# Kernel tuning notes

Hardware: AMD Instinct MI355X
Metric: run time of the kernel (lower is better)

## Reference

```python
import jax, jax.numpy as jnp
import numpy as np

DIM = 128
HID = 128
EPS = 1e-5

def setup_inputs() -> dict:
    key = jax.random.key(0)
    ks = jax.random.split(key, 9)
    s = 1.0 / np.sqrt(DIM)
    sh = 1.0 / np.sqrt(HID)
    return {
        "pair_repr": jax.random.normal(ks[0], (1, 512, 512, DIM), dtype=jnp.float32),
        "Wl": jax.random.uniform(ks[1], (DIM, HID), jnp.float32, -s, s),
        "bl": jax.random.uniform(ks[2], (HID,), jnp.float32, -s, s),
        "Wr": jax.random.uniform(ks[3], (DIM, HID), jnp.float32, -s, s),
        "br": jax.random.uniform(ks[4], (HID,), jnp.float32, -s, s),
        "Wo": jax.random.uniform(ks[5], (HID, DIM), jnp.float32, -sh, sh),
        "bo": jax.random.uniform(ks[6], (DIM,), jnp.float32, -sh, sh),
        "Wg": jax.random.uniform(ks[7], (DIM, DIM), jnp.float32, -s, s),
        "bg": jax.random.uniform(ks[8], (DIM,), jnp.float32, -s, s),
        "gamma": jnp.ones((DIM,), jnp.float32),
        "beta": jnp.zeros((DIM,), jnp.float32),
    }

def reference(pair_repr, Wl, bl, Wr, br, Wo, bo, Wg, bg, gamma, beta):
    # left/right projections: (B, L, L, H)
    left = pair_repr @ Wl + bl
    right = pair_repr @ Wr + br
    # triangle multiplication: out[b,i,j,h] = sum_k left[b,i,k,h] * right[b,k,j,h]
    out = jnp.einsum('bikh,bkjh->bijh', left, right)
    out = out @ Wo + bo
    gate = jax.nn.sigmoid(pair_repr @ Wg + bg)
    out = pair_repr + gate * out
    # LayerNorm over last dim
    mu = jnp.mean(out, axis=-1, keepdims=True)
    var = jnp.mean((out - mu) ** 2, axis=-1, keepdims=True)
    return (out - mu) * jax.lax.rsqrt(var + EPS) * gamma + beta
```

## Files before the change

kernel.cpp:

```cpp
#include <hip/hip_runtime.h>
#include <hip/hip_bf16.h>


#define LSZ 512
#define NPOS (LSZ * LSZ)

typedef short s16;
typedef __attribute__((ext_vector_type(4))) short s16x4;
typedef __attribute__((ext_vector_type(8))) short s16x8;
typedef __attribute__((ext_vector_type(4))) float f32x4;

typedef const __attribute__((address_space(1))) unsigned int* gas1;
typedef __attribute__((address_space(3))) unsigned int* las3;

static __device__ __forceinline__ s16 f2bf(float f) {
    unsigned int u = __builtin_bit_cast(unsigned int, f);
    u += 0x7FFFu + ((u >> 16) & 1u);
    return (s16)(u >> 16);
}

static __device__ __forceinline__ unsigned pkbf(float x, float y) {
    __hip_bfloat162 h = __float22bfloat162_rn(make_float2(x, y));
    unsigned u;
    __builtin_memcpy(&u, &h, 4);
    return u;
}
static __device__ __forceinline__ s16x8 cvt8(f32x4 a, f32x4 b) {
    union { s16x8 v; unsigned u[4]; } r;
    r.u[0] = pkbf(a[0], a[1]);
    r.u[1] = pkbf(a[2], a[3]);
    r.u[2] = pkbf(b[0], b[1]);
    r.u[3] = pkbf(b[2], b[3]);
    return r.v;
}
static __device__ __forceinline__ s16x4 cvt4(float x0, float x1, float x2, float x3) {
    union { s16x4 v; unsigned u[2]; } r;
    r.u[0] = pkbf(x0, x1);
    r.u[1] = pkbf(x2, x3);
    return r.v;
}

static __device__ __forceinline__ void gload_lds16(const void* g, void* l) {
    __builtin_amdgcn_global_load_lds((gas1)g, (las3)l, 16, 0, 0);
}

__global__ void k_prep(const float* __restrict__ Wl, const float* __restrict__ Wr,
                       const float* __restrict__ Wg, const float* __restrict__ Wo,
                       s16* __restrict__ WlT, s16* __restrict__ WrT,
                       s16* __restrict__ WgT, s16* __restrict__ WoT) {
    const float* src;
    s16* dst;
    switch (blockIdx.x) {
        case 0: src = Wl; dst = WlT; break;
        case 1: src = Wr; dst = WrT; break;
        case 2: src = Wg; dst = WgT; break;
        default: src = Wo; dst = WoT; break;
    }
    for (int e = threadIdx.x; e < 128 * 128; e += blockDim.x) {
        int o = e >> 7, i = e & 127;
        dst[e] = f2bf(src[i * 128 + o]);
    }
}

template <int COLMODE>
__global__ __launch_bounds__(256) void k_proj(const float* __restrict__ pair,
                                              const s16* __restrict__ WT,
                                              const float* __restrict__ bias,
                                              s16* __restrict__ outT) {
    __shared__ __align__(16) s16 As[128 * 128];
    const int t = threadIdx.x;
    const int b = blockIdx.x;
    const int c0 = b & 511, rb = b >> 9;
    {
        const int p = t >> 1;
        const int dh = (t & 1) << 6;
        long gpos = COLMODE ? ((long)(rb * 128 + p) * 512 + c0) : ((long)b * 128 + p);
        const float* src = pair + gpos * 128 + dh;
        const int swz = (p & 7) << 4;
        char* lrow = (char*)As + p * 256;
#pragma unroll
        for (int g = 0; g < 8; ++g) {
            f32x4 v0 = *(const f32x4*)(src + g * 8);
            f32x4 v1 = *(const f32x4*)(src + g * 8 + 4);
            s16x8 pk = cvt8(v0, v1);
            *(s16x8*)(lrow + ((dh * 2 + g * 16) ^ swz)) = pk;
        }
    }
    __syncthreads();
    const int w = t >> 6, l = t & 63;
    const int wr = (w >> 1) * 64, wc = (w & 1) * 64;
    const int lr = l & 15, lg = l >> 4;
    f32x4 acc[4][4];
#pragma unroll
    for (int mi = 0; mi < 4; ++mi)
#pragma unroll
        for (int ni = 0; ni < 4; ++ni) acc[mi][ni] = (f32x4){0.f, 0.f, 0.f, 0.f};
#pragma unroll
    for (int ks = 0; ks < 4; ++ks) {
        const int kk = ks * 32 + lg * 8;
        s16x8 af[4], bfv[4];
#pragma unroll
        for (int mi = 0; mi < 4; ++mi) {
            int row = wr + mi * 16 + lr;
            af[mi] = *(const s16x8*)((const char*)As + ((row * 256 + kk * 2) ^ ((row & 7) << 4)));
        }
#pragma unroll
        for (int ni = 0; ni < 4; ++ni) {
            int h = wc + ni * 16 + lr;
            bfv[ni] = *(const s16x8*)(WT + h * 128 + kk);
        }
#pragma unroll
        for (int mi = 0; mi < 4; ++mi)
#pragma unroll
            for (int ni = 0; ni < 4; ++ni)
                acc[mi][ni] = __builtin_amdgcn_mfma_f32_16x16x32_bf16(af[mi], bfv[ni], acc[mi][ni], 0, 0, 0);
    }
#pragma unroll
    for (int ni = 0; ni < 4; ++ni) {
        const int h = wc + ni * 16 + lr;
        const float bv = bias[h];
        long base = (long)h * NPOS + (COLMODE ? ((long)c0 * 512 + rb * 128) : ((long)b * 128));
#pragma unroll
        for (int mi = 0; mi < 4; ++mi) {
            const int prow = wr + mi * 16 + lg * 4;
            s16x4 pk = cvt4(acc[mi][ni][0] + bv, acc[mi][ni][1] + bv,
                            acc[mi][ni][2] + bv, acc[mi][ni][3] + bv);
            *(s16x4*)(outT + base + prow) = pk;
        }
    }
}

__global__ __launch_bounds__(512, 2) void k_tri(const s16* __restrict__ leftT,
                                                const s16* __restrict__ rightTT,
                                                s16* __restrict__ tri) {
    __shared__ __align__(16) s16 As[256 * 64];
    __shared__ __align__(16) s16 Bs[256 * 64];
    const int t = threadIdx.x;
    const int logical = ((blockIdx.x & 7) << 6) | (blockIdx.x >> 3);
    const int h = logical >> 2;
    const int ti = (logical >> 1) & 1, tj = logical & 1;
    const s16* Ap = leftT + (long)h * NPOS + (long)ti * 256 * 512;
    const s16* Bp = rightTT + (long)h * NPOS + (long)tj * 256 * 512;
    const int w = t >> 6, l = t & 63;
    const int wr = (w >> 2) * 128, wc = (w & 3) * 64;
    const int lr = l & 15, lg = l >> 4;
    f32x4 acc[8][4];
#pragma unroll
    for (int mi = 0; mi < 8; ++mi)
#pragma unroll
        for (int ni = 0; ni < 4; ++ni) acc[mi][ni] = (f32x4){0.f, 0.f, 0.f, 0.f};
    for (int kb = 0; kb < 512; kb += 64) {
        __syncthreads();
#pragma unroll
        for (int P = 0; P < 4; ++P) {
            const int unit = P * 512 + t;
            const int row = unit >> 3, u = unit & 7;
            const int kks = (u ^ (row & 7)) << 3;
            gload_lds16(Ap + (long)row * 512 + kb + kks, (char*)As + unit * 16);
            gload_lds16(Bp + (long)row * 512 + kb + kks, (char*)Bs + unit * 16);
        }
        __syncthreads();
#pragma unroll
        for (int ks = 0; ks < 2; ++ks) {
            s16x8 af[8], bfv[4];
#pragma unroll
            for (int mi = 0; mi < 8; ++mi) {
                const int row = wr + mi * 16 + lr;
                af[mi] = *(const s16x8*)((const char*)As + row * 128 + (((ks * 4 + lg) ^ (row & 7)) << 4));
            }
#pragma unroll
            for (int ni = 0; ni < 4; ++ni) {
                const int row = wc + ni * 16 + lr;
                bfv[ni] = *(const s16x8*)((const char*)Bs + row * 128 + (((ks * 4 + lg) ^ (row & 7)) << 4));
            }
#pragma unroll
            for (int mi = 0; mi < 8; ++mi)
#pragma unroll
                for (int ni = 0; ni < 4; ++ni)
                    acc[mi][ni] = __builtin_amdgcn_mfma_f32_16x16x32_bf16(af[mi], bfv[ni], acc[mi][ni], 0, 0, 0);
        }
    }
#pragma unroll
    for (int mi = 0; mi < 8; ++mi) {
#pragma unroll
        for (int r = 0; r < 4; ++r) {
            const int i = ti * 256 + wr + mi * 16 + lg * 4 + r;
            s16* dst = tri + (long)h * NPOS + (long)i * 512 + tj * 256 + wc;
#pragma unroll
            for (int ni = 0; ni < 4; ++ni) dst[ni * 16 + lr] = f2bf(acc[mi][ni][r]);
        }
    }
}

#define WAITVM(N) asm volatile("s_waitcnt vmcnt(" #N ")" ::: "memory")

#define SUBTILE(BUF, SUB) do {                                                        \
    const int row_ = (SUB) * 16 + lr;                                                 \
    const int po_ = row_ >> 3, p3_ = row_ & 7;                                        \
    const char* pbp_ = (const char*)&PA[BUF][0] + row_ * 512;                         \
    f32x4 accO_ = (f32x4){0.f, 0.f, 0.f, 0.f};                                        \
    f32x4 accG_ = (f32x4){0.f, 0.f, 0.f, 0.f};                                        \
    _Pragma("unroll")                                                                 \
    for (int ks = 0; ks < 4; ++ks) {                                                  \
        const int kk = ks * 32 + lg * 8;                                              \
        s16x8 tbv_;                                                                   \
        _Pragma("unroll")                                                             \
        for (int j = 0; j < 8; ++j) {                                                 \
            const int hh_ = kk + j;                                                   \
            tbv_[j] = TRI[BUF][(hh_ * 4 + (po_ ^ ((hh_ >> 3) & 3))) * 8 + p3_];       \
        }                                                                             \
        f32x4 pa0_ = *(const f32x4*)(pbp_ + ((((ks << 3) | (lg << 1)) ^ rsw) << 4));  \
        f32x4 pa1_ = *(const f32x4*)(pbp_ + (((((ks << 3) | (lg << 1)) + 1) ^ rsw) << 4)); \
        s16x8 pf_ = cvt8(pa0_, pa1_);                                                 \
        accO_ = __builtin_amdgcn_mfma_f32_16x16x32_bf16(wo[ks], tbv_, accO_, 0, 0, 0);\
        accG_ = __builtin_amdgcn_mfma_f32_16x16x32_bf16(wg[ks], pf_, accG_, 0, 0, 0); \
    }                                                                                 \
    f32x4 rs_ = *(const f32x4*)(pbp_ + ((((w << 2) | lg) ^ rsw) << 4));               \
    f32x4 xr_;                                                                        \
    _Pragma("unroll")                                                                 \
    for (int r = 0; r < 4; ++r) {                                                     \
        const float gate_ = 1.f / (1.f + __expf(-(accG_[r] + bg4[r])));               \
        xr_[r] = rs_[r] + gate_ * (accO_[r] + bo4[r]);                                \
    }                                                                                 \
    *(f32x4*)&xbuf[row_][dl] = xr_;                                                   \
} while (0)

#define LNPASS(P, META) do {                                                          \
    const int row_ = (P) * 16 + (t >> 5);                                             \
    f32x4 xv_ = *(const f32x4*)&xbuf[row_][lnc];                                      \
    float s_ = xv_[0] + xv_[1] + xv_[2] + xv_[3];                                     \
    s_ += __shfl_xor(s_, 1); s_ += __shfl_xor(s_, 2); s_ += __shfl_xor(s_, 4);        \
    s_ += __shfl_xor(s_, 8); s_ += __shfl_xor(s_, 16);                                \
    const float mu_ = s_ * 0.0078125f;                                                \
    float v_ = 0.f;                                                                   \
    _Pragma("unroll")                                                                 \
    for (int j = 0; j < 4; ++j) { float dd_ = xv_[j] - mu_; v_ += dd_ * dd_; }        \
    v_ += __shfl_xor(v_, 1); v_ += __shfl_xor(v_, 2); v_ += __shfl_xor(v_, 4);        \
    v_ += __shfl_xor(v_, 8); v_ += __shfl_xor(v_, 16);                                \
    const float rstd_ = rsqrtf(v_ * 0.0078125f + 1e-5f);                              \
    f32x4 o_;                                                                         \
    _Pragma("unroll")                                                                 \
    for (int j = 0; j < 4; ++j) o_[j] = (xv_[j] - mu_) * rstd_ * gm4[j] + bt4[j];     \
    *(f32x4*)(out + ((META) * 32 + row_) * 128 + lnc) = o_;                           \
} while (0)

#define ITER(M, NLIT, DOPF) do {                                                      \
    WAITVM(NLIT);                                                                     \
    __builtin_amdgcn_s_barrier();                                                     \
    SUBTILE((M) & 1, 0);                                                              \
    SUBTILE((M) & 1, 1);                                                              \
    asm volatile("s_waitcnt lgkmcnt(0)" ::: "memory");                                \
    __builtin_amdgcn_s_barrier();                                                     \
    __builtin_amdgcn_sched_barrier(0);                                                \
    if (DOPF) stage((M) & 1, meta0 + (M) + 2);                                        \
    LNPASS(0, meta0 + (M));                                                           \
    LNPASS(1, meta0 + (M));                                                           \
} while (0)

__global__ __launch_bounds__(512, 2) void k_final(const float* __restrict__ pair,
                                                  const s16* __restrict__ tri,
                                                  const s16* __restrict__ WgT,
                                                  const s16* __restrict__ WoT,
                                                  const float* __restrict__ bgv,
                                                  const float* __restrict__ bov,
                                                  const float* __restrict__ gam,
                                                  const float* __restrict__ bet,
                                                  float* __restrict__ out) {
    __shared__ __align__(16) s16 TRI[2][32 * 128];
    __shared__ __align__(16) float PA[2][32 * 128];
    __shared__ __align__(16) float xbuf[32][132];
    const int t = threadIdx.x;
    const int w = t >> 6, l = t & 63;
    const int lr = l & 15, lg = l >> 4;
    const int d0 = w << 4;
    const int dl = d0 + (lg << 2);
    const int rsw = lr & 7;
    s16x8 wo[4], wg[4];
#pragma unroll
    for (int ks = 0; ks < 4; ++ks) {
        wo[ks] = *(const s16x8*)(WoT + (d0 + lr) * 128 + ks * 32 + lg * 8);
        wg[ks] = *(const s16x8*)(WgT + (d0 + lr) * 128 + ks * 32 + lg * 8);
    }
    const f32x4 bo4 = *(const f32x4*)(bov + dl);
    const f32x4 bg4 = *(const f32x4*)(bgv + dl);
    const int lnc = (t & 31) << 2;
    const f32x4 gm4 = *(const f32x4*)(gam + lnc);
    const f32x4 bt4 = *(const f32x4*)(bet + lnc);
    const long meta0 = (long)blockIdx.x * 8;

    auto stage = [&](int buf, long meta) {
        const long pb = meta * 32;
        {
            const int hh = t >> 2;
            const int po = (t & 3) ^ ((hh >> 3) & 3);
            gload_lds16(tri + (long)hh * NPOS + pb + po * 8,
                        (char*)&TRI[buf][0] + t * 16);
        }
        {
            const int row = t >> 5, u = t & 31;
            gload_lds16(pair + (pb + row) * 128 + ((u ^ (row & 7)) << 2),
                        (char*)&PA[buf][0] + t * 16);
        }
        {
            const int row = 16 + (t >> 5), u = t & 31;
            gload_lds16(pair + (pb + row) * 128 + ((u ^ (row & 7)) << 2),
                        (char*)&PA[buf][0] + 8192 + t * 16);
        }
    };

    stage(0, meta0 + 0);
    stage(1, meta0 + 1);
    ITER(0, 3, 1);
    ITER(1, 3, 1);
    ITER(2, 3, 1);
    ITER(3, 3, 1);
    ITER(4, 3, 1);
    ITER(5, 3, 1);
    ITER(6, 3, 0);
    ITER(7, 0, 0);
}

extern "C" void kernel_launch(void* const* d_in, const int* in_sizes, int n_in,
                              void* d_out, int out_size, void* d_ws, size_t ws_size,
                              hipStream_t stream) {
    const float* pair = (const float*)d_in[0];
    const float* Wl   = (const float*)d_in[1];
    const float* bl   = (const float*)d_in[2];
    const float* Wr   = (const float*)d_in[3];
    const float* br   = (const float*)d_in[4];
    const float* Wo   = (const float*)d_in[5];
    const float* bo   = (const float*)d_in[6];
    const float* Wg   = (const float*)d_in[7];
    const float* bg   = (const float*)d_in[8];
    const float* gam  = (const float*)d_in[9];
    const float* bet  = (const float*)d_in[10];
    float* out = (float*)d_out;

    s16* WlT = (s16*)d_ws;
    s16* WrT = WlT + 128 * 128;
    s16* WgT = WrT + 128 * 128;
    s16* WoT = WgT + 128 * 128;
    s16* leftT   = WoT + 128 * 128;
    s16* rightTT = leftT + (long)128 * NPOS;
    s16* tri     = rightTT + (long)128 * NPOS;

    k_prep<<<4, 256, 0, stream>>>(Wl, Wr, Wg, Wo, WlT, WrT, WgT, WoT);
    k_proj<0><<<2048, 256, 0, stream>>>(pair, WlT, bl, leftT);
    k_proj<1><<<2048, 256, 0, stream>>>(pair, WrT, br, rightTT);
    k_tri<<<512, 512, 0, stream>>>(leftT, rightTT, tri);
    k_final<<<1024, 512, 0, stream>>>(pair, tri, WgT, WoT, bg, bo, gam, bet, out);
}
```

Before: 281.4 us.

## Pipeline projection kernel with double-buffered async global-to-LDS loads

Rewrites k_proj so each 512-thread block walks 8 tiles of 32 positions, streaming fp32 pair rows straight into swizzled LDS with global_load_lds and double buffering, while weight fragments stay in registers. Each wave computes 16 output channels, converting fp32 to bf16 at fragment-read time, and writes transposed outputs. The aim is to overlap the global load of the input with MFMA work and to drop the staging convert-and-store pass. In exchange, output stores become scalar 2-byte writes, which may coalesce less well, and the explicit barrier and waitcnt choreography is fragile.

```diff
diff --git a/kernel.cpp b/kernel.cpp
--- a/kernel.cpp
+++ b/kernel.cpp
@@ -43,6 +43,8 @@
 static __device__ __forceinline__ void gload_lds16(const void* g, void* l) {
     __builtin_amdgcn_global_load_lds((gas1)g, (las3)l, 16, 0, 0);
 }
+
+#define WAITVM(N) asm volatile("s_waitcnt vmcnt(" #N ")" ::: "memory")
 
 __global__ void k_prep(const float* __restrict__ Wl, const float* __restrict__ Wr,
                        const float* __restrict__ Wg, const float* __restrict__ Wo,
@@ -62,72 +64,81 @@
     }
 }
 
+#define PSUB(BUF, SUB, META) do {                                                     \
+    const int row_ = (SUB) * 16 + lr;                                                 \
+    const char* pbp_ = (const char*)&PA[BUF][0] + row_ * 512;                         \
+    f32x4 acc_ = (f32x4){0.f, 0.f, 0.f, 0.f};                                         \
+    _Pragma("unroll")                                                                 \
+    for (int ks = 0; ks < 4; ++ks) {                                                  \
+        f32x4 pa0_ = *(const f32x4*)(pbp_ + ((((ks << 3) | (lg << 1)) ^ rsw) << 4));  \
+        f32x4 pa1_ = *(const f32x4*)(pbp_ + (((((ks << 3) | (lg << 1)) + 1) ^ rsw) << 4)); \
+        s16x8 pf_ = cvt8(pa0_, pa1_);                                                 \
+        acc_ = __builtin_amdgcn_mfma_f32_16x16x32_bf16(wv[ks], pf_, acc_, 0, 0, 0);   \
+    }                                                                                 \
+    const long pbase_ = COLMODE ? ((long)((META) >> 4) * 512 + (((META) & 15) << 5) + row_) \
+                                : ((long)(META) * 32 + row_);                         \
+    _Pragma("unroll")                                                                 \
+    for (int r = 0; r < 4; ++r)                                                       \
+        outT[(long)(dl + r) * NPOS + pbase_] = f2bf(acc_[r] + b4[r]);                 \
+} while (0)
+
+#define PITER(M, NLIT, DOPF) do {                                                     \
+    WAITVM(NLIT);                                                                     \
+    __builtin_amdgcn_s_barrier();                                                     \
+    PSUB((M) & 1, 0, meta0 + (M));                                                    \
+    PSUB((M) & 1, 1, meta0 + (M));                                                    \
+    asm volatile("s_waitcnt lgkmcnt(0)" ::: "memory");                                \
+    __builtin_amdgcn_s_barrier();                                                     \
+    __builtin_amdgcn_sched_barrier(0);                                                \
+    if (DOPF) stage((M) & 1, meta0 + (M) + 2);                                        \
+} while (0)
+
 template <int COLMODE>
-__global__ __launch_bounds__(256) void k_proj(const float* __restrict__ pair,
-                                              const s16* __restrict__ WT,
-                                              const float* __restrict__ bias,
-                                              s16* __restrict__ outT) {
-    __shared__ __align__(16) s16 As[128 * 128];
+__global__ __launch_bounds__(512, 4) void k_proj(const float* __restrict__ pair,
+                                                 const s16* __restrict__ WT,
+                                                 const float* __restrict__ bias,
+                                                 s16* __restrict__ outT) {
+    __shared__ __align__(16) float PA[2][32 * 128];
     const int t = threadIdx.x;
-    const int b = blockIdx.x;
-    const int c0 = b & 511, rb = b >> 9;
-    {
-        const int p = t >> 1;
-        const int dh = (t & 1) << 6;
-        long gpos = COLMODE ? ((long)(rb * 128 + p) * 512 + c0) : ((long)b * 128 + p);
-        const float* src = pair + gpos * 128 + dh;
-        const int swz = (p & 7) << 4;
-        char* lrow = (char*)As + p * 256;
-#pragma unroll
-        for (int g = 0; g < 8; ++g) {
-            f32x4 v0 = *(const f32x4*)(src + g * 8);
-            f32x4 v1 = *(const f32x4*)(src + g * 8 + 4);
-            s16x8 pk = cvt8(v0, v1);
-            *(s16x8*)(lrow + ((dh * 2 + g * 16) ^ swz)) = pk;
-        }
-    }
-    __syncthreads();
     const int w = t >> 6, l = t & 63;
-    const int wr = (w >> 1) * 64, wc = (w & 1) * 64;
     const int lr = l & 15, lg = l >> 4;
-    f32x4 acc[4][4];
-#pragma unroll
-    for (int mi = 0; mi < 4; ++mi)
-#pragma unroll
-        for (int ni = 0; ni < 4; ++ni) acc[mi][ni] = (f32x4){0.f, 0.f, 0.f, 0.f};
-#pragma unroll
-    for (int ks = 0; ks < 4; ++ks) {
-        const int kk = ks * 32 + lg * 8;
-        s16x8 af[4], bfv[4];
-#pragma unroll
-        for (int mi = 0; mi < 4; ++mi) {
-            int row = wr + mi * 16 + lr;
-            af[mi] = *(const s16x8*)((const char*)As + ((row * 256 + kk * 2) ^ ((row & 7) << 4)));
-        }
-#pragma unroll
-        for (int ni = 0; ni < 4; ++ni) {
-            int h = wc + ni * 16 + lr;
-            bfv[ni] = *(const s16x8*)(WT + h * 128 + kk);
-        }
-#pragma unroll
-        for (int mi = 0; mi < 4; ++mi)
-#pragma unroll
-            for (int ni = 0; ni < 4; ++ni)
-                acc[mi][ni] = __builtin_amdgcn_mfma_f32_16x16x32_bf16(af[mi], bfv[ni], acc[mi][ni], 0, 0, 0);
-    }
-#pragma unroll
-    for (int ni = 0; ni < 4; ++ni) {
-        const int h = wc + ni * 16 + lr;
-        const float bv = bias[h];
-        long base = (long)h * NPOS + (COLMODE ? ((long)c0 * 512 + rb * 128) : ((long)b * 128));
-#pragma unroll
-        for (int mi = 0; mi < 4; ++mi) {
-            const int prow = wr + mi * 16 + lg * 4;
-            s16x4 pk = cvt4(acc[mi][ni][0] + bv, acc[mi][ni][1] + bv,
-                            acc[mi][ni][2] + bv, acc[mi][ni][3] + bv);
-            *(s16x4*)(outT + base + prow) = pk;
-        }
-    }
+    const int d0 = w << 4;
+    const int dl = d0 + (lg << 2);
+    const int rsw = lr & 7;
+    s16x8 wv[4];
+#pragma unroll
+    for (int ks = 0; ks < 4; ++ks)
+        wv[ks] = *(const s16x8*)(WT + (d0 + lr) * 128 + ks * 32 + lg * 8);
+    const f32x4 b4 = *(const f32x4*)(bias + dl);
+    const long meta0 = (long)blockIdx.x * 8;
+
+    auto stage = [&](int buf, long meta) {
+        {
+            const int row = t >> 5, u = t & 31;
+            const long gp = COLMODE ? (((meta & 15) * 32 + row) * 512 + (meta >> 4))
+                                    : (meta * 32 + row);
+            gload_lds16(pair + gp * 128 + ((u ^ (row & 7)) << 2),
+                        (char*)&PA[buf][0] + t * 16);
+        }
+        {
+            const int row = 16 + (t >> 5), u = t & 31;
+            const long gp = COLMODE ? (((meta & 15) * 32 + row) * 512 + (meta >> 4))
+                                    : (meta * 32 + row);
+            gload_lds16(pair + gp * 128 + ((u ^ (row & 7)) << 2),
+                        (char*)&PA[buf][0] + 8192 + t * 16);
+        }
+    };
+
+    stage(0, meta0 + 0);
+    stage(1, meta0 + 1);
+    PITER(0, 2, 1);
+    PITER(1, 2, 1);
+    PITER(2, 2, 1);
+    PITER(3, 2, 1);
+    PITER(4, 2, 1);
+    PITER(5, 2, 1);
+    PITER(6, 2, 0);
+    PITER(7, 0, 0);
 }
 
 __global__ __launch_bounds__(512, 2) void k_tri(const s16* __restrict__ leftT,
@@ -191,8 +202,6 @@
         }
     }
 }
-
-#define WAITVM(N) asm volatile("s_waitcnt vmcnt(" #N ")" ::: "memory")
 
 #define SUBTILE(BUF, SUB) do {                                                        \
     const int row_ = (SUB) * 16 + lr;                                                 \
@@ -345,8 +354,8 @@
     s16* tri     = rightTT + (long)128 * NPOS;
 
     k_prep<<<4, 256, 0, stream>>>(Wl, Wr, Wg, Wo, WlT, WrT, WgT, WoT);
-    k_proj<0><<<2048, 256, 0, stream>>>(pair, WlT, bl, leftT);
-    k_proj<1><<<2048, 256, 0, stream>>>(pair, WrT, br, rightTT);
+    k_proj<0><<<1024, 512, 0, stream>>>(pair, WlT, bl, leftT);
+    k_proj<1><<<1024, 512, 0, stream>>>(pair, WrT, br, rightTT);
     k_tri<<<512, 512, 0, stream>>>(leftT, rightTT, tri);
     k_final<<<1024, 512, 0, stream>>>(pair, tri, WgT, WoT, bg, bo, gam, bet, out);
 }
```

Result: faster. 254.6 us (-9.5%).
